# Optimization experiments

Measured on AMD Instinct MI355X. Metric: run time of the kernel, lower is better.

Reference implementation:

```python
import jax, jax.numpy as jnp
import numpy as np

NUM_FREQS = 12  # fourfeat_config
EMB_DIM = 3 + 6 * NUM_FREQS  # identity + sin/cos per freq per dim = 75


def fourier_ipe(x, cov, decay):
    # x: [N,3], cov: [N,3,3], decay: scalar (coarse-to-fine window cutoff)
    N = x.shape[0]
    freqs = 2.0 ** jnp.arange(NUM_FREQS, dtype=jnp.float32)            # [F]
    xb = x[:, None, :] * freqs[:, None]                                # [N,F,3]
    var = jnp.diagonal(cov, axis1=-2, axis2=-1)[:, None, :] * (freqs ** 2)[:, None]  # [N,F,3]
    # nerfies-style cosine easing window per frequency band
    window = 0.5 * (1.0 - jnp.cos(jnp.pi * jnp.clip(decay - jnp.arange(NUM_FREQS, dtype=jnp.float32), 0.0, 1.0)))  # [F]
    atten = jnp.exp(-0.5 * var) * window[:, None]                      # [N,F,3]
    four = jnp.concatenate([jnp.sin(xb), jnp.cos(xb)], axis=-1) * jnp.concatenate([atten, atten], axis=-1)  # [N,F,6]
    return jnp.concatenate([x, four.reshape(N, 6 * NUM_FREQS)], axis=-1)  # [N,75]


def mlp(h, W_in, b_in, W_hid, b_hid, W_out, b_out):
    h = jax.nn.relu(h @ W_in + b_in)
    for i in range(W_hid.shape[0]):  # fixed small layer count
        h = jax.nn.relu(h @ W_hid[i] + b_hid[i])
    return h @ W_out + b_out  # output_activation = None


def setup_inputs() -> dict:
    key = jax.random.key(0)
    ks = jax.random.split(key, 16)
    bshape = (2, 16384, 8)
    mean = jax.random.normal(ks[0], (*bshape, 3), jnp.float32)
    cov = jax.random.uniform(ks[1], (*bshape, 3, 3), jnp.float32) * 1e-4  # small positive diag

    def w(k, shp):
        return jax.random.normal(k, shp, jnp.float32) / np.sqrt(shp[-2]).astype(np.float32)

    FD, FC = 256, 128  # features_density, features_color
    HD, HC = 8 - 2, 4 - 2  # n_hidden_layers = layers - 2
    return {
        'mean': mean, 'cov': cov,
        'Wd_in': w(ks[2], (EMB_DIM, FD)), 'bd_in': jnp.zeros((FD,), jnp.float32),
        'Wd_hid': w(ks[3], (HD, FD, FD)), 'bd_hid': jnp.zeros((HD, FD), jnp.float32),
        'Wd_out': w(ks[4], (FD, FD + 1)), 'bd_out': jnp.zeros((FD + 1,), jnp.float32),
        'Wc_in': w(ks[5], (FD, FC)), 'bc_in': jnp.zeros((FC,), jnp.float32),
        'Wc_hid': w(ks[6], (HC, FC, FC)), 'bc_hid': jnp.zeros((HC, FC), jnp.float32),
        'Wc_out': w(ks[7], (FC, 3)), 'bc_out': jnp.zeros((3,), jnp.float32),
        'decayscale': 12,
    }


def reference(mean, cov, Wd_in, bd_in, Wd_hid, bd_hid, Wd_out, bd_out,
              Wc_in, bc_in, Wc_hid, bc_hid, Wc_out, bc_out, decayscale):
    batch_shape = mean.shape[:-1]
    N = int(np.prod(batch_shape))
    x = mean.reshape(N, 3)
    c = cov.reshape(N, 3, 3)
    emb = fourier_ipe(x, c, jnp.float32(decayscale))                    # [N,75]
    feat = mlp(emb, Wd_in, bd_in, Wd_hid, bd_hid, Wd_out, bd_out)       # [N,257]
    d, features = feat[:, :1], feat[:, 1:]
    # parameterization == 'VolSDF' (capitalized) -> no SDF radius offset branch
    raw_rgb = mlp(features, Wc_in, bc_in, Wc_hid, bc_hid, Wc_out, bc_out)  # [N,3]
    raw = jnp.concatenate([raw_rgb, d], axis=-1)                        # [N,4]
    return raw.reshape(*batch_shape, 4)
```

## Files before the change

### kernel.cpp

```cpp
#include <hip/hip_runtime.h>
#include <hip/hip_bf16.h>

#define PI_F 3.14159265358979323846f
#define KPAD 260

typedef _Float16 h8 __attribute__((ext_vector_type(8)));
typedef _Float16 h4 __attribute__((ext_vector_type(4)));
typedef _Float16 h2 __attribute__((ext_vector_type(2)));
typedef __fp16 fp16x2 __attribute__((ext_vector_type(2)));
typedef float f32x16 __attribute__((ext_vector_type(16)));

__device__ __forceinline__ h2 cvt_pk_h2(float a, float b)
{
    fp16x2 r = __builtin_amdgcn_cvt_pkrtz(a, b);
    return __builtin_bit_cast(h2, r);
}

#define OFF_DIN   0
#define OFF_DHID  24576
#define OFF_FEAT  417792
#define OFF_CIN   483328
#define OFF_CHID  516096
#define OFF_COUT  548864
#define W_TOTAL   552960
#define FB_DIN  0
#define FB_DHID 256
#define FB_FEAT 1792
#define FB_CIN  2048
#define FB_CHID 2176
#define FB_WD0  2432
#define FB_BD0  2688
#define B_TOTAL 2689
#define PREP_TOTAL (W_TOTAL + B_TOTAL)

__global__ void prep_kernel(const float* __restrict__ Wd_in,  const float* __restrict__ Wd_hid,
                            const float* __restrict__ Wd_out, const float* __restrict__ Wc_in,
                            const float* __restrict__ Wc_hid, const float* __restrict__ Wc_out,
                            const float* __restrict__ bd_in,  const float* __restrict__ bd_hid,
                            const float* __restrict__ bd_out, const float* __restrict__ bc_in,
                            const float* __restrict__ bc_hid,
                            _Float16* __restrict__ wdst, float* __restrict__ bdst)
{
    int i = blockIdx.x * 256 + threadIdx.x;
    if (i >= PREP_TOTAL) return;
    if (i < W_TOTAL) {
        float v = 0.f;
        int j, n, k;
        #define DECODE(jj, KTv)  do { int frag = (jj) >> 3; int e = (jj) & 7;          \
                                      int lane = frag & 63; int tk = frag >> 6;         \
                                      int ntl = tk / (KTv); int kt = tk % (KTv);        \
                                      n = ntl * 32 + (lane & 31);                       \
                                      k = kt * 16 + (lane >> 5) * 8 + e; } while (0)
        if (i < OFF_DHID) {
            j = i; DECODE(j, 6);
            if (k < 75) v = Wd_in[k * 256 + n];
        } else if (i < OFF_FEAT) {
            j = i - OFF_DHID; int l = j >> 16; j &= 65535; DECODE(j, 16);
            v = Wd_hid[(l * 256 + k) * 256 + n];
        } else if (i < OFF_CIN) {
            j = i - OFF_FEAT; DECODE(j, 16);
            v = Wd_out[k * 257 + n + 1];
        } else if (i < OFF_CHID) {
            j = i - OFF_CIN; DECODE(j, 16);
            v = Wc_in[k * 128 + n];
        } else if (i < OFF_COUT) {
            j = i - OFF_CHID; int l = j >> 14; j &= 16383; DECODE(j, 8);
            v = Wc_hid[(l * 128 + k) * 128 + n];
        } else {
            j = i - OFF_COUT; DECODE(j, 8);
            if (n < 3) v = Wc_out[k * 3 + n];
        }
        #undef DECODE
        wdst[i] = (_Float16)v;
    } else {
        int b = i - W_TOTAL;
        float v = 0.f;
        #define BDECODE(bb) int ntl = (bb) >> 5; int r5 = (bb) & 31;                   \
                            int lq = r5 >> 4, jj = r5 & 15;                            \
                            int n = ntl * 32 + (jj & 3) + 8 * (jj >> 2) + 4 * lq
        if (b < FB_DHID)      { BDECODE(b); v = bd_in[n]; }
        else if (b < FB_FEAT) { int b2 = b - FB_DHID; int l = b2 >> 8; int bb = b2 & 255;
                                BDECODE(bb); v = bd_hid[l * 256 + n]; }
        else if (b < FB_CIN)  { int bb = b - FB_FEAT; BDECODE(bb); v = bd_out[n + 1]; }
        else if (b < FB_CHID) { int bb = b - FB_CIN; BDECODE(bb); v = bc_in[n]; }
        else if (b < FB_WD0)  { int b2 = b - FB_CHID; int l = b2 >> 7; int bb = b2 & 127;
                                BDECODE(bb); v = bc_hid[l * 128 + n]; }
        else if (b < FB_BD0)  { int k = b - FB_WD0; v = Wd_out[k * 257]; }
        else                  { v = bd_out[0]; }
        #undef BDECODE
        bdst[b] = v;
    }
}

__device__ __forceinline__ h8 lds_read_h8(const _Float16* p)
{
    h4 lo = *(const h4*)(p);
    h4 hi = *(const h4*)(p + 4);
    return __builtin_shufflevector(lo, hi, 0, 1, 2, 3, 4, 5, 6, 7);
}

template<int KT, int NT, bool RELU, bool DDOT>
__device__ __forceinline__ void dense(_Float16 (*At)[KPAD],
                                      const _Float16* __restrict__ WP,
                                      const float* __restrict__ bfrag,
                                      const float* __restrict__ wd0,
                                      float (*dpart)[128],
                                      int rbase, int ntile0, int wid,
                                      int lrow, int lq, int lane)
{
    f32x16 acc[2][NT];
#pragma unroll
    for (int nt = 0; nt < NT; ++nt) {
        f32x16 b = *(const f32x16*)(bfrag + (ntile0 + nt) * 32 + lq * 16);
        acc[0][nt] = b;
        acc[1][nt] = b;
    }

    const _Float16* wbase = WP + ((size_t)ntile0 * KT) * 512 + (size_t)lane * 8;

#pragma unroll 2
    for (int kt = 0; kt < KT; ++kt) {
        const int koff = kt * 16 + lq * 8;
        h8 wf[NT];
#pragma unroll
        for (int nt = 0; nt < NT; ++nt)
            wf[nt] = *(const h8*)(wbase + (size_t)(nt * KT + kt) * 512);
        h8 af[2];
#pragma unroll
        for (int mt = 0; mt < 2; ++mt)
            af[mt] = lds_read_h8(&At[rbase + mt * 32 + lrow][koff]);
        __builtin_amdgcn_s_setprio(1);
#pragma unroll
        for (int mt = 0; mt < 2; ++mt)
#pragma unroll
            for (int nt = 0; nt < NT; ++nt)
                acc[mt][nt] = __builtin_amdgcn_mfma_f32_32x32x16_f16(wf[nt], af[mt], acc[mt][nt], 0, 0, 0);
        __builtin_amdgcn_s_setprio(0);
    }

    if (DDOT) {
        const float* w0 = wd0 + wid * 64;
#pragma unroll
        for (int m2 = 0; m2 < 2; ++m2) {
            const int m = lane + m2 * 64;
            float s = 0.f;
#pragma unroll
            for (int kk = 0; kk < 64; kk += 8) {
                h8 hv = lds_read_h8(&At[m][wid * 64 + kk]);
#pragma unroll
                for (int e = 0; e < 8; ++e)
                    s = fmaf((float)hv[e], w0[kk + e], s);
            }
            dpart[wid][m] = s;
        }
    }

    __syncthreads();

#pragma unroll
    for (int mt = 0; mt < 2; ++mt) {
        const int m = rbase + mt * 32 + lrow;
#pragma unroll
        for (int nt = 0; nt < NT; ++nt) {
#pragma unroll
            for (int p = 0; p < 4; ++p) {
                const int n0 = (ntile0 + nt) * 32 + p * 8 + lq * 4;
                h2 lo = cvt_pk_h2(acc[mt][nt][4 * p + 0], acc[mt][nt][4 * p + 1]);
                h2 hi = cvt_pk_h2(acc[mt][nt][4 * p + 2], acc[mt][nt][4 * p + 3]);
                h4 hv = __builtin_shufflevector(lo, hi, 0, 1, 2, 3);
                if (RELU) {
                    const h4 zero = {(_Float16)0, (_Float16)0, (_Float16)0, (_Float16)0};
                    hv = __builtin_elementwise_max(hv, zero);
                }
                *(h4*)(&At[m][n0]) = hv;
            }
        }
    }
    __syncthreads();
}

__global__ __launch_bounds__(256, 2)
void ffmlp_kernel(const float* __restrict__ mean, const float* __restrict__ cov,
                  const int* __restrict__ decayscale,
                  const _Float16* __restrict__ wws, const float* __restrict__ bws,
                  const float* __restrict__ bc_out,
                  float* __restrict__ out, int N)
{
    __shared__ __align__(16) _Float16 At[128][KPAD];
    __shared__ float dpart[4][128];

    const int t = threadIdx.x;
    const int wid = t >> 6, lane = t & 63;
    const int r = wid >> 1, c = wid & 1;
    const int lrow = lane & 31, lq = lane >> 5;
    const int rbase = r * 64;
    const int p0 = blockIdx.x * 128;

    {
        const int m = t >> 1, hf = t & 1;
        const long pt = (long)p0 + m;
        float x0 = 0.f, x1 = 0.f, x2 = 0.f, v0 = 0.f, v1 = 0.f, v2 = 0.f;
        if (pt < N) {
            x0 = mean[pt * 3 + 0]; x1 = mean[pt * 3 + 1]; x2 = mean[pt * 3 + 2];
            v0 = cov[pt * 9 + 0];  v1 = cov[pt * 9 + 4];  v2 = cov[pt * 9 + 8];
        }
        const float dec = (float)(*decayscale);
        if (hf == 0) {
            At[m][0] = (_Float16)x0; At[m][1] = (_Float16)x1; At[m][2] = (_Float16)x2;
            for (int k = 75; k < 86; ++k) At[m][k] = (_Float16)0.f;
        } else {
            for (int k = 86; k < 96; ++k) At[m][k] = (_Float16)0.f;
        }
        const float xs[3] = {x0, x1, x2}, vs[3] = {v0, v1, v2};
#pragma unroll
        for (int fi = 0; fi < 6; ++fi) {
            const int f = hf * 6 + fi;
            const float fs = (float)(1 << f);
            const float wcl = fminf(fmaxf(dec - (float)f, 0.f), 1.f);
            const float win = 0.5f * (1.f - cosf(wcl * PI_F));
#pragma unroll
            for (int d = 0; d < 3; ++d) {
                const float xb = xs[d] * fs;
                const float att = expf(-0.5f * vs[d] * fs * fs) * win;
                float s, co;
                sincosf(xb, &s, &co);
                At[m][3 + 6 * f + d] = (_Float16)(s * att);
                At[m][6 + 6 * f + d] = (_Float16)(co * att);
            }
        }
    }
    __syncthreads();

    dense<6, 4, true, false>(At, wws + OFF_DIN, bws + FB_DIN, bws, dpart,
                             rbase, c * 4, wid, lrow, lq, lane);
#pragma unroll 1
    for (int i = 0; i < 6; ++i)
        dense<16, 4, true, false>(At, wws + OFF_DHID + i * 65536, bws + FB_DHID + i * 256,
                                  bws, dpart, rbase, c * 4, wid, lrow, lq, lane);
    dense<16, 4, false, true>(At, wws + OFF_FEAT, bws + FB_FEAT, bws + FB_WD0, dpart,
                              rbase, c * 4, wid, lrow, lq, lane);

    dense<16, 2, true, false>(At, wws + OFF_CIN, bws + FB_CIN, bws, dpart,
                              rbase, c * 2, wid, lrow, lq, lane);
#pragma unroll 1
    for (int i = 0; i < 2; ++i)
        dense<8, 2, true, false>(At, wws + OFF_CHID + i * 16384, bws + FB_CHID + i * 128,
                                 bws, dpart, rbase, c * 2, wid, lrow, lq, lane);

    if (c == 0) {
        f32x16 acc[2];
#pragma unroll
        for (int mt = 0; mt < 2; ++mt)
#pragma unroll
            for (int j = 0; j < 16; ++j) acc[mt][j] = 0.f;
        const _Float16* wco = wws + OFF_COUT + (size_t)lane * 8;
#pragma unroll
        for (int kt = 0; kt < 8; ++kt) {
            const int koff = kt * 16 + lq * 8;
            h8 wf = *(const h8*)(wco + (size_t)kt * 512);
#pragma unroll
            for (int mt = 0; mt < 2; ++mt) {
                h8 af = lds_read_h8(&At[rbase + mt * 32 + lrow][koff]);
                acc[mt] = __builtin_amdgcn_mfma_f32_32x32x16_f16(wf, af, acc[mt], 0, 0, 0);
            }
        }
        const float bc0 = bc_out[0], bc1 = bc_out[1], bc2 = bc_out[2];
        const float bd0 = bws[FB_BD0];
        if (lq == 0) {
#pragma unroll
            for (int mt = 0; mt < 2; ++mt) {
                const int m = rbase + mt * 32 + lrow;
                const long pt = (long)p0 + m;
                if (pt < N) {
                    float4 o;
                    o.x = acc[mt][0] + bc0;
                    o.y = acc[mt][1] + bc1;
                    o.z = acc[mt][2] + bc2;
                    o.w = dpart[0][m] + dpart[1][m] + dpart[2][m] + dpart[3][m] + bd0;
                    *(float4*)(out + pt * 4) = o;
                }
            }
        }
    }
}

extern "C" void kernel_launch(void* const* d_in, const int* in_sizes, int n_in,
                              void* d_out, int out_size, void* d_ws, size_t ws_size,
                              hipStream_t stream)
{
    const float* mean   = (const float*)d_in[0];
    const float* cov    = (const float*)d_in[1];
    const float* Wd_in  = (const float*)d_in[2];
    const float* bd_in  = (const float*)d_in[3];
    const float* Wd_hid = (const float*)d_in[4];
    const float* bd_hid = (const float*)d_in[5];
    const float* Wd_out = (const float*)d_in[6];
    const float* bd_out = (const float*)d_in[7];
    const float* Wc_in  = (const float*)d_in[8];
    const float* bc_in  = (const float*)d_in[9];
    const float* Wc_hid = (const float*)d_in[10];
    const float* bc_hid = (const float*)d_in[11];
    const float* Wc_out = (const float*)d_in[12];
    const float* bc_out = (const float*)d_in[13];
    const int*   decay  = (const int*)d_in[14];

    _Float16* wws = (_Float16*)d_ws;
    float*    bws = (float*)((char*)d_ws + (size_t)W_TOTAL * 2);

    const int N = in_sizes[0] / 3;

    const int prep_blocks = (PREP_TOTAL + 255) / 256;
    prep_kernel<<<prep_blocks, 256, 0, stream>>>(Wd_in, Wd_hid, Wd_out, Wc_in, Wc_hid, Wc_out,
                                                 bd_in, bd_hid, bd_out, bc_in, bc_hid, wws, bws);

    const int blocks = (N + 127) / 128;
    ffmlp_kernel<<<blocks, 256, 0, stream>>>(mean, cov, decay, wws, bws, bc_out, (float*)d_out, N);
}
```

Baseline: 307.1 us.

## Enlarge block to 256 points with 8 waves, each computing 4x2 MFMA tiles

The fused MLP kernel now processes 256 points per block with 512 threads (8 waves in a 2x4 grid). Each wave computes 128 rows by fewer column tiles, so every weight fragment read from global memory is reused across four row tiles instead of two. The goal is to halve weight traffic per point. In exchange the block needs about 141 KB of dynamic LDS and more accumulator registers per wave, which may limit occupancy, and the density dot product is now split across 8 waves.

```diff
diff --git a/kernel.cpp b/kernel.cpp
--- a/kernel.cpp
+++ b/kernel.cpp
@@ -99,21 +99,22 @@
     return __builtin_shufflevector(lo, hi, 0, 1, 2, 3, 4, 5, 6, 7);
 }
 
-template<int KT, int NT, bool RELU, bool DDOT>
+template<int KT, int NT, int MT, bool RELU, bool DDOT>
 __device__ __forceinline__ void dense(_Float16 (*At)[KPAD],
                                       const _Float16* __restrict__ WP,
                                       const float* __restrict__ bfrag,
                                       const float* __restrict__ wd0,
-                                      float (*dpart)[128],
+                                      float (*dpart)[256],
                                       int rbase, int ntile0, int wid,
                                       int lrow, int lq, int lane)
 {
-    f32x16 acc[2][NT];
+    f32x16 acc[MT][NT];
 #pragma unroll
     for (int nt = 0; nt < NT; ++nt) {
         f32x16 b = *(const f32x16*)(bfrag + (ntile0 + nt) * 32 + lq * 16);
-        acc[0][nt] = b;
-        acc[1][nt] = b;
+#pragma unroll
+        for (int mt = 0; mt < MT; ++mt)
+            acc[mt][nt] = b;
     }
 
     const _Float16* wbase = WP + ((size_t)ntile0 * KT) * 512 + (size_t)lane * 8;
@@ -125,13 +126,13 @@
 #pragma unroll
         for (int nt = 0; nt < NT; ++nt)
             wf[nt] = *(const h8*)(wbase + (size_t)(nt * KT + kt) * 512);
-        h8 af[2];
-#pragma unroll
-        for (int mt = 0; mt < 2; ++mt)
+        h8 af[MT];
+#pragma unroll
+        for (int mt = 0; mt < MT; ++mt)
             af[mt] = lds_read_h8(&At[rbase + mt * 32 + lrow][koff]);
         __builtin_amdgcn_s_setprio(1);
 #pragma unroll
-        for (int mt = 0; mt < 2; ++mt)
+        for (int mt = 0; mt < MT; ++mt)
 #pragma unroll
             for (int nt = 0; nt < NT; ++nt)
                 acc[mt][nt] = __builtin_amdgcn_mfma_f32_32x32x16_f16(wf[nt], af[mt], acc[mt][nt], 0, 0, 0);
@@ -139,14 +140,14 @@
     }
 
     if (DDOT) {
-        const float* w0 = wd0 + wid * 64;
-#pragma unroll
-        for (int m2 = 0; m2 < 2; ++m2) {
+        const float* w0 = wd0 + wid * 32;
+#pragma unroll
+        for (int m2 = 0; m2 < 4; ++m2) {
             const int m = lane + m2 * 64;
             float s = 0.f;
 #pragma unroll
-            for (int kk = 0; kk < 64; kk += 8) {
-                h8 hv = lds_read_h8(&At[m][wid * 64 + kk]);
+            for (int kk = 0; kk < 32; kk += 8) {
+                h8 hv = lds_read_h8(&At[m][wid * 32 + kk]);
 #pragma unroll
                 for (int e = 0; e < 8; ++e)
                     s = fmaf((float)hv[e], w0[kk + e], s);
@@ -158,7 +159,7 @@
     __syncthreads();
 
 #pragma unroll
-    for (int mt = 0; mt < 2; ++mt) {
+    for (int mt = 0; mt < MT; ++mt) {
         const int m = rbase + mt * 32 + lrow;
 #pragma unroll
         for (int nt = 0; nt < NT; ++nt) {
@@ -179,22 +180,23 @@
     __syncthreads();
 }
 
-__global__ __launch_bounds__(256, 2)
+__global__ __launch_bounds__(512, 2)
 void ffmlp_kernel(const float* __restrict__ mean, const float* __restrict__ cov,
                   const int* __restrict__ decayscale,
                   const _Float16* __restrict__ wws, const float* __restrict__ bws,
                   const float* __restrict__ bc_out,
                   float* __restrict__ out, int N)
 {
-    __shared__ __align__(16) _Float16 At[128][KPAD];
-    __shared__ float dpart[4][128];
+    extern __shared__ __align__(16) char smem[];
+    _Float16 (*At)[KPAD] = (_Float16 (*)[KPAD])smem;
+    float (*dpart)[256]  = (float (*)[256])(smem + 256 * KPAD * 2);
 
     const int t = threadIdx.x;
     const int wid = t >> 6, lane = t & 63;
-    const int r = wid >> 1, c = wid & 1;
+    const int r = wid >> 2, c = wid & 3;
     const int lrow = lane & 31, lq = lane >> 5;
-    const int rbase = r * 64;
-    const int p0 = blockIdx.x * 128;
+    const int rbase = r * 128;
+    const int p0 = blockIdx.x * 256;
 
     {
         const int m = t >> 1, hf = t & 1;
@@ -231,26 +233,26 @@
     }
     __syncthreads();
 
-    dense<6, 4, true, false>(At, wws + OFF_DIN, bws + FB_DIN, bws, dpart,
-                             rbase, c * 4, wid, lrow, lq, lane);
+    dense<6, 2, 4, true, false>(At, wws + OFF_DIN, bws + FB_DIN, bws, dpart,
+                                rbase, c * 2, wid, lrow, lq, lane);
 #pragma unroll 1
     for (int i = 0; i < 6; ++i)
-        dense<16, 4, true, false>(At, wws + OFF_DHID + i * 65536, bws + FB_DHID + i * 256,
-                                  bws, dpart, rbase, c * 4, wid, lrow, lq, lane);
-    dense<16, 4, false, true>(At, wws + OFF_FEAT, bws + FB_FEAT, bws + FB_WD0, dpart,
-                              rbase, c * 4, wid, lrow, lq, lane);
-
-    dense<16, 2, true, false>(At, wws + OFF_CIN, bws + FB_CIN, bws, dpart,
-                              rbase, c * 2, wid, lrow, lq, lane);
+        dense<16, 2, 4, true, false>(At, wws + OFF_DHID + i * 65536, bws + FB_DHID + i * 256,
+                                     bws, dpart, rbase, c * 2, wid, lrow, lq, lane);
+    dense<16, 2, 4, false, true>(At, wws + OFF_FEAT, bws + FB_FEAT, bws + FB_WD0, dpart,
+                                 rbase, c * 2, wid, lrow, lq, lane);
+
+    dense<16, 1, 4, true, false>(At, wws + OFF_CIN, bws + FB_CIN, bws, dpart,
+                                 rbase, c, wid, lrow, lq, lane);
 #pragma unroll 1
     for (int i = 0; i < 2; ++i)
-        dense<8, 2, true, false>(At, wws + OFF_CHID + i * 16384, bws + FB_CHID + i * 128,
-                                 bws, dpart, rbase, c * 2, wid, lrow, lq, lane);
+        dense<8, 1, 4, true, false>(At, wws + OFF_CHID + i * 16384, bws + FB_CHID + i * 128,
+                                    bws, dpart, rbase, c, wid, lrow, lq, lane);
 
     if (c == 0) {
-        f32x16 acc[2];
-#pragma unroll
-        for (int mt = 0; mt < 2; ++mt)
+        f32x16 acc[4];
+#pragma unroll
+        for (int mt = 0; mt < 4; ++mt)
 #pragma unroll
             for (int j = 0; j < 16; ++j) acc[mt][j] = 0.f;
         const _Float16* wco = wws + OFF_COUT + (size_t)lane * 8;
@@ -259,7 +261,7 @@
             const int koff = kt * 16 + lq * 8;
             h8 wf = *(const h8*)(wco + (size_t)kt * 512);
 #pragma unroll
-            for (int mt = 0; mt < 2; ++mt) {
+            for (int mt = 0; mt < 4; ++mt) {
                 h8 af = lds_read_h8(&At[rbase + mt * 32 + lrow][koff]);
                 acc[mt] = __builtin_amdgcn_mfma_f32_32x32x16_f16(wf, af, acc[mt], 0, 0, 0);
             }
@@ -268,21 +270,26 @@
         const float bd0 = bws[FB_BD0];
         if (lq == 0) {
 #pragma unroll
-            for (int mt = 0; mt < 2; ++mt) {
+            for (int mt = 0; mt < 4; ++mt) {
                 const int m = rbase + mt * 32 + lrow;
                 const long pt = (long)p0 + m;
                 if (pt < N) {
+                    float dsum = bd0;
+#pragma unroll
+                    for (int w = 0; w < 8; ++w) dsum += dpart[w][m];
                     float4 o;
                     o.x = acc[mt][0] + bc0;
                     o.y = acc[mt][1] + bc1;
                     o.z = acc[mt][2] + bc2;
-                    o.w = dpart[0][m] + dpart[1][m] + dpart[2][m] + dpart[3][m] + bd0;
+                    o.w = dsum;
                     *(float4*)(out + pt * 4) = o;
                 }
             }
         }
     }
 }
+
+#define LDS_BYTES (256 * KPAD * 2 + 8 * 256 * 4)
 
 extern "C" void kernel_launch(void* const* d_in, const int* in_sizes, int n_in,
                               void* d_out, int out_size, void* d_ws, size_t ws_size,
@@ -309,10 +316,18 @@
 
     const int N = in_sizes[0] / 3;
 
+    static bool attr_set = false;
+    if (!attr_set) {
+        (void)hipFuncSetAttribute((const void*)ffmlp_kernel,
+                                  hipFuncAttributeMaxDynamicSharedMemorySize, LDS_BYTES);
+        attr_set = true;
+    }
+
     const int prep_blocks = (PREP_TOTAL + 255) / 256;
     prep_kernel<<<prep_blocks, 256, 0, stream>>>(Wd_in, Wd_hid, Wd_out, Wc_in, Wc_hid, Wc_out,
                                                  bd_in, bd_hid, bd_out, bc_in, bc_hid, wws, bws);
 
-    const int blocks = (N + 127) / 128;
-    ffmlp_kernel<<<blocks, 256, 0, stream>>>(mean, cov, decay, wws, bws, bc_out, (float*)d_out, N);
-}
+    const int blocks = (N + 255) / 256;
+    ffmlp_kernel<<<blocks, 512, LDS_BYTES, stream>>>(mean, cov, decay, wws, bws, bc_out,
+                                                     (float*)d_out, N);
+}
```

New measurement: 320.3 us. 1.04x slower.
